# Optimization experiments

Measured on AMD Instinct MI355X. Metric: run time of the kernel, lower is better.

Reference implementation:

```python
import jax, jax.numpy as jnp
import numpy as np

H = 8
DQ = 32
DK = 32
DV = 32
DC = DQ + DK  # concat dim for additive attention


def setup_inputs() -> dict:
    key = jax.random.key(0)
    ks = jax.random.split(key, 8)
    bs, Lq, Lk = 2, 384, 384
    q = jax.random.normal(ks[0], (bs, Lq, H * DQ), jnp.float32)
    k = jax.random.normal(ks[1], (bs, Lk, H * DK), jnp.float32)
    v = jax.random.normal(ks[2], (bs, Lk, H * DV), jnp.float32)
    q_sequence_lengths = jax.random.randint(ks[3], (bs,), 1, Lq + 1, dtype=jnp.int32)
    k_sequence_lengths = jax.random.randint(ks[4], (bs,), 1, Lk + 1, dtype=jnp.int32)
    bound = 1.0 / np.sqrt(DC)
    w1 = jax.random.uniform(ks[5], (H, DC, DC), jnp.float32, -bound, bound)
    b1 = jax.random.uniform(ks[6], (H, DC), jnp.float32, -bound, bound)
    w2 = jax.random.uniform(ks[7], (H, DC), jnp.float32, -1.0, 1.0)
    return {"q": q, "k": k, "v": v,
            "q_sequence_lengths": q_sequence_lengths,
            "k_sequence_lengths": k_sequence_lengths,
            "w1": w1, "b1": b1, "w2": w2}


def reference(q, k, v, q_sequence_lengths, k_sequence_lengths, w1, b1, w2):
    bs, Lq, _ = q.shape
    Lk = k.shape[1]
    # split heads: (b, h, L, d)
    qh = q.reshape(bs, Lq, H, DQ).transpose(0, 2, 1, 3)
    kh = k.reshape(bs, Lk, H, DK).transpose(0, 2, 1, 3)
    vh = v.reshape(bs, Lk, H, DV).transpose(0, 2, 1, 3)
    # additive scores: tanh(cat(q_i, k_j) @ W1 + b1) @ w2
    # cat @ W1 == q @ W1[:DQ] + k @ W1[DQ:]  (avoids materializing the cat)
    qW = jnp.einsum('bhqd,hde->bhqe', qh, w1[:, :DQ, :])
    kW = jnp.einsum('bhkd,hde->bhke', kh, w1[:, DQ:, :])
    hid = jnp.tanh(qW[:, :, :, None, :] + kW[:, :, None, :, :] + b1[None, :, None, None, :])  # (b,h,q,k,DC)
    scores = jnp.einsum('bhqke,he->bhqk', hid, w2)
    # key-side length mask (end padded)
    kmask = jnp.arange(Lk)[None, :] < k_sequence_lengths[:, None]  # (b, Lk)
    scores = jnp.where(kmask[:, None, None, :], scores, jnp.float32(-1e9))
    att = jax.nn.softmax(scores, axis=-1)  # (b,h,q,k)
    out = jnp.einsum('bhqk,bhkd->bqhd', att, vh)  # (b,q,h,DV)
    # query-side length mask zeros out padded query rows
    qmask = jnp.arange(Lq)[None, :] < q_sequence_lengths[:, None]  # (b, Lq)
    out = out * qmask[:, :, None, None].astype(out.dtype)
    return out.reshape(bs, Lq, H * DV), att
```

## Files before the change

### kernel.cpp

```cpp
#include <hip/hip_runtime.h>

#define NH 8
#define LQ 384
#define LK 384
#define BS 2

typedef float v4f __attribute__((ext_vector_type(4)));
__device__ __forceinline__ v4f fma4(v4f a, v4f b, v4f c) { return __builtin_elementwise_fma(a, b, c); }
__device__ __forceinline__ v4f sp4(float x) { v4f r; r.x = x; r.y = x; r.z = x; r.w = x; return r; }

__global__ __launch_bounds__(256) void pre_ek_kernel(
    const float* __restrict__ kin, const float* __restrict__ w1,
    const float* __restrict__ b1, float* __restrict__ ws)
{
    __shared__ float tile[16][65];
    const int bid = blockIdx.x;
    const int bh = bid / 24, kt = bid % 24;
    const int b = bh >> 3, h = bh & 7;
    const int k0 = kt * 16;
    const int tid = threadIdx.x;
    const int lane = tid & 63, w = tid >> 6;

    float w1c[32];
    const float* w1p = w1 + (size_t)(h * 64 + 32) * 64 + lane;
    #pragma unroll
    for (int d = 0; d < 32; ++d) w1c[d] = w1p[d * 64];
    const float bv = b1[h * 64 + lane];

    #pragma unroll
    for (int s = 0; s < 4; ++s) {
        int kr = w * 4 + s;
        const float* krow = kin + ((size_t)(b * LK + k0 + kr)) * (NH * 32) + h * 32;
        float acc = bv;
        #pragma unroll
        for (int d = 0; d < 32; ++d) acc = __builtin_fmaf(krow[d], w1c[d], acc);
        tile[kr][lane] = __expf(acc + acc);
    }
    __syncthreads();
    {
        int e4 = tid >> 4, k16 = tid & 15;
        float4 o;
        o.x = tile[k16][e4 * 4 + 0];
        o.y = tile[k16][e4 * 4 + 1];
        o.z = tile[k16][e4 * 4 + 2];
        o.w = tile[k16][e4 * 4 + 3];
        ((float4*)ws)[((size_t)(bh * 16 + e4)) * LK + k0 + k16] = o;
    }
}

__global__ __launch_bounds__(256) void attn_kernel(
    const float* __restrict__ qin, const float* __restrict__ vin,
    const int* __restrict__ qlens, const int* __restrict__ klens,
    const float* __restrict__ w1, const float* __restrict__ w2g,
    const float* __restrict__ ws,
    float* __restrict__ outg, float* __restrict__ attg)
{
    __shared__ __align__(16) float eqi_s[2][256];
    __shared__ __align__(16) float att_h[4][4 * 192];
    __shared__ __align__(16) float w2s[64];
    __shared__ float2 smu[2][4][2];
    __shared__ __align__(16) float4 pvp[2][2][4][8];

    const int tid = threadIdx.x, wave = tid >> 6, lane = tid & 63;
    const int pair = wave >> 1, hh = wave & 1;
    const int bh = blockIdx.x / 48, tile = blockIdx.x % 48;
    const int b = bh >> 3, h = bh & 7;
    const int q0 = tile * 8;
    const int klen = klens[b], qlen = qlens[b];

    {
        float w1c[32];
        const float* w1p = w1 + (size_t)h * 64 * 64 + lane;
        #pragma unroll
        for (int d = 0; d < 32; ++d) w1c[d] = w1p[d * 64];
        #pragma unroll
        for (int j = 0; j < 2; ++j) {
            int r = wave * 2 + j;
            const float* qp = qin + ((size_t)(b * LQ + q0 + r)) * (NH * 32) + h * 32;
            float a = 0.f;
            #pragma unroll
            for (int d = 0; d < 32; ++d) a = __builtin_fmaf(qp[d], w1c[d], a);
            eqi_s[r >> 2][lane * 4 + (r & 3)] = __expf(a + a);
        }
        if (wave == 0) w2s[lane] = w2g[h * 64 + lane];
    }
    __syncthreads();

    v4f sc[3];
    sc[0] = sp4(0.f); sc[1] = sp4(0.f); sc[2] = sp4(0.f);
    const float4* ekq = (const float4*)ws + ((size_t)bh * 16) * LK + hh * 192 + lane;
    const v4f*   eqp = (const v4f*)eqi_s[pair];
    const float4* w2p = (const float4*)w2s;

    float4 kva[3], kvb[3];
    #pragma unroll
    for (int c = 0; c < 3; ++c) kva[c] = ekq[c * 64];
    #pragma unroll
    for (int c = 0; c < 3; ++c) kvb[c] = ekq[LK + c * 64];

    #pragma unroll
    for (int p = 0; p < 8; ++p) {
        const int ea = 2 * p, eb = 2 * p + 1;
        float4 As[3] = {kva[0], kva[1], kva[2]};
        float4 Bs[3] = {kvb[0], kvb[1], kvb[2]};
        if (p < 7) {
            const float4* np = ekq + (size_t)(ea + 2) * LK;
            kva[0] = np[0]; kva[1] = np[64]; kva[2] = np[128];
            const float4* nq = ekq + (size_t)(eb + 2) * LK;
            kvb[0] = nq[0]; kvb[1] = nq[64]; kvb[2] = nq[128];
        }
        v4f Ea0 = eqp[ea * 4 + 0];
        v4f Ea1 = eqp[ea * 4 + 1];
        v4f Ea2 = eqp[ea * 4 + 2];
        v4f Ea3 = eqp[ea * 4 + 3];
        v4f Eb0 = eqp[eb * 4 + 0];
        v4f Eb1 = eqp[eb * 4 + 1];
        v4f Eb2 = eqp[eb * 4 + 2];
        v4f Eb3 = eqp[eb * 4 + 3];
        float4 wva = w2p[ea], wvb = w2p[eb];
        #pragma unroll
        for (int c = 0; c < 3; ++c) {
            float4 ka = As[c], kb = Bs[c];
            v4f ta0 = fma4(Ea0, sp4(ka.x), sp4(1.f));
            v4f ta1 = fma4(Ea1, sp4(ka.y), sp4(1.f));
            v4f ta2 = fma4(Ea2, sp4(ka.z), sp4(1.f));
            v4f ta3 = fma4(Ea3, sp4(ka.w), sp4(1.f));
            v4f pa12 = ta0 * ta1, pa34 = ta2 * ta3;
            v4f na12 = fma4(sp4(wva.y), ta0, sp4(wva.x) * ta1);
            v4f na34 = fma4(sp4(wva.w), ta2, sp4(wva.z) * ta3);
            v4f numA = fma4(na34, pa12, na12 * pa34);
            v4f denA = pa12 * pa34;
            v4f tb0 = fma4(Eb0, sp4(kb.x), sp4(1.f));
            v4f tb1 = fma4(Eb1, sp4(kb.y), sp4(1.f));
            v4f tb2 = fma4(Eb2, sp4(kb.z), sp4(1.f));
            v4f tb3 = fma4(Eb3, sp4(kb.w), sp4(1.f));
            v4f pb12 = tb0 * tb1, pb34 = tb2 * tb3;
            v4f nb12 = fma4(sp4(wvb.y), tb0, sp4(wvb.x) * tb1);
            v4f nb34 = fma4(sp4(wvb.w), tb2, sp4(wvb.z) * tb3);
            v4f numB = fma4(nb34, pb12, nb12 * pb34);
            v4f denB = pb12 * pb34;
            v4f num = fma4(numB, denA, numA * denB);
            v4f den = denA * denB;
            v4f r;
            r.x = __builtin_amdgcn_rcpf(den.x);
            r.y = __builtin_amdgcn_rcpf(den.y);
            r.z = __builtin_amdgcn_rcpf(den.z);
            r.w = __builtin_amdgcn_rcpf(den.w);
            sc[c] = fma4(num, r, sc[c]);
        }
    }

    float s_[3][4];
    float m_[4] = {-3.4e38f, -3.4e38f, -3.4e38f, -3.4e38f};
    #pragma unroll
    for (int c = 0; c < 3; ++c) {
        int kk = hh * 192 + c * 64 + lane;
        bool ok = kk < klen;
        #pragma unroll
        for (int r = 0; r < 4; ++r) {
            s_[c][r] = ok ? -2.0f * sc[c][r] : -3.4e38f;
            m_[r] = fmaxf(m_[r], s_[c][r]);
        }
    }
    #pragma unroll
    for (int off = 32; off >= 1; off >>= 1) {
        #pragma unroll
        for (int r = 0; r < 4; ++r) m_[r] = fmaxf(m_[r], __shfl_xor(m_[r], off));
    }
    float e_[3][4];
    float u_[4] = {0.f, 0.f, 0.f, 0.f};
    #pragma unroll
    for (int c = 0; c < 3; ++c) {
        int kk = hh * 192 + c * 64 + lane;
        bool ok = kk < klen;
        #pragma unroll
        for (int r = 0; r < 4; ++r) {
            e_[c][r] = ok ? __expf(s_[c][r] - m_[r]) : 0.f;
            u_[r] += e_[c][r];
        }
    }
    #pragma unroll
    for (int off = 32; off >= 1; off >>= 1) {
        #pragma unroll
        for (int r = 0; r < 4; ++r) u_[r] += __shfl_xor(u_[r], off);
    }
    if (lane == 0) {
        #pragma unroll
        for (int r = 0; r < 4; ++r) smu[pair][r][hh] = make_float2(m_[r], u_[r]);
    }
    {
        float* ar = att_h[wave];
        #pragma unroll
        for (int c = 0; c < 3; ++c)
            #pragma unroll
            for (int r = 0; r < 4; ++r)
                ar[r * 192 + c * 64 + lane] = e_[c][r];
    }

    const int kf = lane >> 3, dg = lane & 7;
    const float* vbase = vin + (size_t)b * LK * (NH * 32) + h * 32
                       + (size_t)(hh * 192 + kf) * (NH * 32) + dg * 4;
    const float* ap = att_h[wave];
    float oa[4][4] = {{0.f,0.f,0.f,0.f},{0.f,0.f,0.f,0.f},{0.f,0.f,0.f,0.f},{0.f,0.f,0.f,0.f}};
    float4 vbuf[2];
    vbuf[0] = *(const float4*)(vbase);
    vbuf[1] = *(const float4*)(vbase + (size_t)8 * (NH * 32));
    #pragma unroll
    for (int i = 0; i < 24; ++i) {
        float4 vv = vbuf[i & 1];
        if (i < 22) vbuf[i & 1] = *(const float4*)(vbase + (size_t)((i + 2) * 8) * (NH * 32));
        int k0 = i * 8;
        #pragma unroll
        for (int r = 0; r < 4; ++r) {
            float a = ap[r * 192 + k0 + kf];
            oa[r][0] = __builtin_fmaf(a, vv.x, oa[r][0]);
            oa[r][1] = __builtin_fmaf(a, vv.y, oa[r][1]);
            oa[r][2] = __builtin_fmaf(a, vv.z, oa[r][2]);
            oa[r][3] = __builtin_fmaf(a, vv.w, oa[r][3]);
        }
    }
    #pragma unroll
    for (int r = 0; r < 4; ++r)
        #pragma unroll
        for (int u = 0; u < 4; ++u) {
            oa[r][u] += __shfl_xor(oa[r][u], 8);
            oa[r][u] += __shfl_xor(oa[r][u], 16);
            oa[r][u] += __shfl_xor(oa[r][u], 32);
        }
    __syncthreads();

    float f_[4];
    #pragma unroll
    for (int r = 0; r < 4; ++r) {
        float2 A = smu[pair][r][0], B = smu[pair][r][1];
        float mm = fmaxf(A.x, B.x);
        float uu = A.y * __expf(A.x - mm) + B.y * __expf(B.x - mm);
        f_[r] = __expf(m_[r] - mm) * __builtin_amdgcn_rcpf(uu);
    }

    if (kf == 0) {
        #pragma unroll
        for (int r = 0; r < 4; ++r)
            pvp[pair][hh][r][dg] = make_float4(oa[r][0] * f_[r], oa[r][1] * f_[r],
                                               oa[r][2] * f_[r], oa[r][3] * f_[r]);
    }
    __syncthreads();

    if (lane < 16) {
        int r = wave * 2 + (lane >> 3);
        int dgo = lane & 7;
        int q = q0 + r;
        float4 xa = pvp[r >> 2][0][r & 3][dgo];
        float4 xb = pvp[r >> 2][1][r & 3][dgo];
        float4 o4;
        bool ok = (q < qlen);
        o4.x = ok ? (xa.x + xb.x) : 0.f;
        o4.y = ok ? (xa.y + xb.y) : 0.f;
        o4.z = ok ? (xa.z + xb.z) : 0.f;
        o4.w = ok ? (xa.w + xb.w) : 0.f;
        ((float4*)(outg + ((size_t)(b * LQ + q)) * (NH * 32) + h * 32))[dgo] = o4;
    }

    {
        float* ag = attg + ((size_t)(bh * LQ + q0 + pair * 4)) * LK + hh * 192;
        #pragma unroll
        for (int r = 0; r < 4; ++r) {
            #pragma unroll
            for (int c = 0; c < 3; ++c) ag[c * 64 + lane] = e_[c][r] * f_[r];
            ag += LK;
        }
    }
}

extern "C" void kernel_launch(void* const* d_in, const int* in_sizes, int n_in,
                              void* d_out, int out_size, void* d_ws, size_t ws_size,
                              hipStream_t stream) {
    const float* q    = (const float*)d_in[0];
    const float* k    = (const float*)d_in[1];
    const float* v    = (const float*)d_in[2];
    const int*   qlen = (const int*)d_in[3];
    const int*   klen = (const int*)d_in[4];
    const float* w1   = (const float*)d_in[5];
    const float* b1   = (const float*)d_in[6];
    const float* w2   = (const float*)d_in[7];
    float* out = (float*)d_out;
    float* att = out + (size_t)BS * LQ * NH * 32;
    float* ws  = (float*)d_ws;

    pre_ek_kernel<<<384, 256, 0, stream>>>(k, w1, b1, ws);
    attn_kernel<<<768, 256, 0, stream>>>(q, v, qlen, klen, w1, w2, ws, out, att);
}
```

Measured before the change: 93.74 us.

## Split key range across three waves per row group with 384-thread blocks

The attention kernel now uses 6 waves per block instead of 4. Each pair of query rows splits the key range into three 128-key chunks rather than two 192-key chunks, so each wave carries less work and fewer registers. The softmax merge and the output reduction are extended to three partial results, and the attention-matrix store is moved before the final barrier. This gives more parallelism and latency hiding, at the cost of more cross-wave merging and a larger block size.

```diff
diff --git a/kernel.cpp b/kernel.cpp
--- a/kernel.cpp
+++ b/kernel.cpp
@@ -48,7 +48,7 @@
     }
 }
 
-__global__ __launch_bounds__(256) void attn_kernel(
+__global__ __launch_bounds__(384, 5) void attn_kernel(
     const float* __restrict__ qin, const float* __restrict__ vin,
     const int* __restrict__ qlens, const int* __restrict__ klens,
     const float* __restrict__ w1, const float* __restrict__ w2g,
@@ -56,19 +56,19 @@
     float* __restrict__ outg, float* __restrict__ attg)
 {
     __shared__ __align__(16) float eqi_s[2][256];
-    __shared__ __align__(16) float att_h[4][4 * 192];
+    __shared__ __align__(16) float att_h[6][4 * 128];
     __shared__ __align__(16) float w2s[64];
-    __shared__ float2 smu[2][4][2];
-    __shared__ __align__(16) float4 pvp[2][2][4][8];
+    __shared__ float2 smu[2][4][3];
+    __shared__ __align__(16) float4 pvp[2][3][4][8];
 
     const int tid = threadIdx.x, wave = tid >> 6, lane = tid & 63;
-    const int pair = wave >> 1, hh = wave & 1;
+    const int pair = wave & 1, t = wave >> 1;
     const int bh = blockIdx.x / 48, tile = blockIdx.x % 48;
     const int b = bh >> 3, h = bh & 7;
     const int q0 = tile * 8;
     const int klen = klens[b], qlen = qlens[b];
 
-    {
+    if (wave < 4) {
         float w1c[32];
         const float* w1p = w1 + (size_t)h * 64 * 64 + lane;
         #pragma unroll
@@ -82,32 +82,33 @@
             for (int d = 0; d < 32; ++d) a = __builtin_fmaf(qp[d], w1c[d], a);
             eqi_s[r >> 2][lane * 4 + (r & 3)] = __expf(a + a);
         }
-        if (wave == 0) w2s[lane] = w2g[h * 64 + lane];
-    }
-    __syncthreads();
-
-    v4f sc[3];
-    sc[0] = sp4(0.f); sc[1] = sp4(0.f); sc[2] = sp4(0.f);
-    const float4* ekq = (const float4*)ws + ((size_t)bh * 16) * LK + hh * 192 + lane;
+    } else if (wave == 4) {
+        w2s[lane] = w2g[h * 64 + lane];
+    }
+    __syncthreads();
+
+    v4f sc[2];
+    sc[0] = sp4(0.f); sc[1] = sp4(0.f);
+    const float4* ekq = (const float4*)ws + ((size_t)bh * 16) * LK + t * 128 + lane;
     const v4f*   eqp = (const v4f*)eqi_s[pair];
     const float4* w2p = (const float4*)w2s;
 
-    float4 kva[3], kvb[3];
-    #pragma unroll
-    for (int c = 0; c < 3; ++c) kva[c] = ekq[c * 64];
-    #pragma unroll
-    for (int c = 0; c < 3; ++c) kvb[c] = ekq[LK + c * 64];
+    float4 kva[2], kvb[2];
+    #pragma unroll
+    for (int c = 0; c < 2; ++c) kva[c] = ekq[c * 64];
+    #pragma unroll
+    for (int c = 0; c < 2; ++c) kvb[c] = ekq[LK + c * 64];
 
     #pragma unroll
     for (int p = 0; p < 8; ++p) {
         const int ea = 2 * p, eb = 2 * p + 1;
-        float4 As[3] = {kva[0], kva[1], kva[2]};
-        float4 Bs[3] = {kvb[0], kvb[1], kvb[2]};
+        float4 As[2] = {kva[0], kva[1]};
+        float4 Bs[2] = {kvb[0], kvb[1]};
         if (p < 7) {
             const float4* np = ekq + (size_t)(ea + 2) * LK;
-            kva[0] = np[0]; kva[1] = np[64]; kva[2] = np[128];
+            kva[0] = np[0]; kva[1] = np[64];
             const float4* nq = ekq + (size_t)(eb + 2) * LK;
-            kvb[0] = nq[0]; kvb[1] = nq[64]; kvb[2] = nq[128];
+            kvb[0] = nq[0]; kvb[1] = nq[64];
         }
         v4f Ea0 = eqp[ea * 4 + 0];
         v4f Ea1 = eqp[ea * 4 + 1];
@@ -119,7 +120,7 @@
         v4f Eb3 = eqp[eb * 4 + 3];
         float4 wva = w2p[ea], wvb = w2p[eb];
         #pragma unroll
-        for (int c = 0; c < 3; ++c) {
+        for (int c = 0; c < 2; ++c) {
             float4 ka = As[c], kb = Bs[c];
             v4f ta0 = fma4(Ea0, sp4(ka.x), sp4(1.f));
             v4f ta1 = fma4(Ea1, sp4(ka.y), sp4(1.f));
@@ -150,11 +151,11 @@
         }
     }
 
-    float s_[3][4];
+    float s_[2][4];
     float m_[4] = {-3.4e38f, -3.4e38f, -3.4e38f, -3.4e38f};
     #pragma unroll
-    for (int c = 0; c < 3; ++c) {
-        int kk = hh * 192 + c * 64 + lane;
+    for (int c = 0; c < 2; ++c) {
+        int kk = t * 128 + c * 64 + lane;
         bool ok = kk < klen;
         #pragma unroll
         for (int r = 0; r < 4; ++r) {
@@ -167,11 +168,11 @@
         #pragma unroll
         for (int r = 0; r < 4; ++r) m_[r] = fmaxf(m_[r], __shfl_xor(m_[r], off));
     }
-    float e_[3][4];
+    float e_[2][4];
     float u_[4] = {0.f, 0.f, 0.f, 0.f};
     #pragma unroll
-    for (int c = 0; c < 3; ++c) {
-        int kk = hh * 192 + c * 64 + lane;
+    for (int c = 0; c < 2; ++c) {
+        int kk = t * 128 + c * 64 + lane;
         bool ok = kk < klen;
         #pragma unroll
         for (int r = 0; r < 4; ++r) {
@@ -186,33 +187,33 @@
     }
     if (lane == 0) {
         #pragma unroll
-        for (int r = 0; r < 4; ++r) smu[pair][r][hh] = make_float2(m_[r], u_[r]);
+        for (int r = 0; r < 4; ++r) smu[pair][r][t] = make_float2(m_[r], u_[r]);
     }
     {
         float* ar = att_h[wave];
         #pragma unroll
-        for (int c = 0; c < 3; ++c)
+        for (int c = 0; c < 2; ++c)
             #pragma unroll
             for (int r = 0; r < 4; ++r)
-                ar[r * 192 + c * 64 + lane] = e_[c][r];
+                ar[r * 128 + c * 64 + lane] = e_[c][r];
     }
 
     const int kf = lane >> 3, dg = lane & 7;
     const float* vbase = vin + (size_t)b * LK * (NH * 32) + h * 32
-                       + (size_t)(hh * 192 + kf) * (NH * 32) + dg * 4;
+                       + (size_t)(t * 128 + kf) * (NH * 32) + dg * 4;
     const float* ap = att_h[wave];
     float oa[4][4] = {{0.f,0.f,0.f,0.f},{0.f,0.f,0.f,0.f},{0.f,0.f,0.f,0.f},{0.f,0.f,0.f,0.f}};
     float4 vbuf[2];
     vbuf[0] = *(const float4*)(vbase);
     vbuf[1] = *(const float4*)(vbase + (size_t)8 * (NH * 32));
     #pragma unroll
-    for (int i = 0; i < 24; ++i) {
+    for (int i = 0; i < 16; ++i) {
         float4 vv = vbuf[i & 1];
-        if (i < 22) vbuf[i & 1] = *(const float4*)(vbase + (size_t)((i + 2) * 8) * (NH * 32));
+        if (i < 14) vbuf[i & 1] = *(const float4*)(vbase + (size_t)((i + 2) * 8) * (NH * 32));
         int k0 = i * 8;
         #pragma unroll
         for (int r = 0; r < 4; ++r) {
-            float a = ap[r * 192 + k0 + kf];
+            float a = ap[r * 128 + k0 + kf];
             oa[r][0] = __builtin_fmaf(a, vv.x, oa[r][0]);
             oa[r][1] = __builtin_fmaf(a, vv.y, oa[r][1]);
             oa[r][2] = __builtin_fmaf(a, vv.z, oa[r][2]);
@@ -232,43 +233,42 @@
     float f_[4];
     #pragma unroll
     for (int r = 0; r < 4; ++r) {
-        float2 A = smu[pair][r][0], B = smu[pair][r][1];
-        float mm = fmaxf(A.x, B.x);
-        float uu = A.y * __expf(A.x - mm) + B.y * __expf(B.x - mm);
+        float2 A = smu[pair][r][0], B = smu[pair][r][1], C = smu[pair][r][2];
+        float mm = fmaxf(fmaxf(A.x, B.x), C.x);
+        float uu = A.y * __expf(A.x - mm) + B.y * __expf(B.x - mm) + C.y * __expf(C.x - mm);
         f_[r] = __expf(m_[r] - mm) * __builtin_amdgcn_rcpf(uu);
     }
 
     if (kf == 0) {
         #pragma unroll
         for (int r = 0; r < 4; ++r)
-            pvp[pair][hh][r][dg] = make_float4(oa[r][0] * f_[r], oa[r][1] * f_[r],
-                                               oa[r][2] * f_[r], oa[r][3] * f_[r]);
-    }
-    __syncthreads();
-
-    if (lane < 16) {
-        int r = wave * 2 + (lane >> 3);
-        int dgo = lane & 7;
+            pvp[pair][t][r][dg] = make_float4(oa[r][0] * f_[r], oa[r][1] * f_[r],
+                                              oa[r][2] * f_[r], oa[r][3] * f_[r]);
+    }
+
+    {
+        float* ag = attg + ((size_t)(bh * LQ + q0 + pair * 4)) * LK + t * 128;
+        #pragma unroll
+        for (int r = 0; r < 4; ++r) {
+            #pragma unroll
+            for (int c = 0; c < 2; ++c) ag[c * 64 + lane] = e_[c][r] * f_[r];
+            ag += LK;
+        }
+    }
+    __syncthreads();
+
+    if (wave == 0) {
+        int r = lane >> 3, dgo = lane & 7;
+        int pr = r >> 2, rr = r & 3;
+        float4 x0 = pvp[pr][0][rr][dgo], x1 = pvp[pr][1][rr][dgo], x2 = pvp[pr][2][rr][dgo];
         int q = q0 + r;
-        float4 xa = pvp[r >> 2][0][r & 3][dgo];
-        float4 xb = pvp[r >> 2][1][r & 3][dgo];
+        bool okq = (q < qlen);
         float4 o4;
-        bool ok = (q < qlen);
-        o4.x = ok ? (xa.x + xb.x) : 0.f;
-        o4.y = ok ? (xa.y + xb.y) : 0.f;
-        o4.z = ok ? (xa.z + xb.z) : 0.f;
-        o4.w = ok ? (xa.w + xb.w) : 0.f;
+        o4.x = okq ? (x0.x + x1.x + x2.x) : 0.f;
+        o4.y = okq ? (x0.y + x1.y + x2.y) : 0.f;
+        o4.z = okq ? (x0.z + x1.z + x2.z) : 0.f;
+        o4.w = okq ? (x0.w + x1.w + x2.w) : 0.f;
         ((float4*)(outg + ((size_t)(b * LQ + q)) * (NH * 32) + h * 32))[dgo] = o4;
-    }
-
-    {
-        float* ag = attg + ((size_t)(bh * LQ + q0 + pair * 4)) * LK + hh * 192;
-        #pragma unroll
-        for (int r = 0; r < 4; ++r) {
-            #pragma unroll
-            for (int c = 0; c < 3; ++c) ag[c * 64 + lane] = e_[c][r] * f_[r];
-            ag += LK;
-        }
     }
 }
 
@@ -288,5 +288,5 @@
     float* ws  = (float*)d_ws;
 
     pre_ek_kernel<<<384, 256, 0, stream>>>(k, w1, b1, ws);
-    attn_kernel<<<768, 256, 0, stream>>>(q, v, qlen, klen, w1, w2, ws, out, att);
+    attn_kernel<<<768, 384, 0, stream>>>(q, v, qlen, klen, w1, w2, ws, out, att);
 }
```

New measurement: 101.3 us. 8.0% more time.
